# Performance work log

Measured on AMD Instinct MI355X. Metric: run time of the kernel, lower is better.

## Reference

```python
import jax, jax.numpy as jnp
import numpy as np

N_LAYERS = 4
D_MODEL = 256
N_HEADS = 8
D_FF = 2 * D_MODEL
EPS_ATTN = 1e-6
EPS_LN = 1e-5


def setup_inputs() -> dict:
    key = jax.random.key(0)
    ks = jax.random.split(key, 20)
    C, F, L = D_MODEL, D_FF, N_LAYERS
    s = 0.02
    return {
        "ref_feature": jax.random.normal(ks[0], (4, C, 128, 128), jnp.float32),
        # per-layer stacked params (torch nn.Linear convention: y = x @ W.T + b)
        "Wq": jax.random.normal(ks[1], (L, C, C), jnp.float32) * s,
        "bq": jnp.zeros((L, C), jnp.float32),
        "Wk": jax.random.normal(ks[2], (L, C, C), jnp.float32) * s,
        "bk": jnp.zeros((L, C), jnp.float32),
        "Wv": jax.random.normal(ks[3], (L, C, C), jnp.float32) * s,
        "bv": jnp.zeros((L, C), jnp.float32),
        "Wo": jax.random.normal(ks[4], (L, C, C), jnp.float32) * s,
        "bo": jnp.zeros((L, C), jnp.float32),
        "g1": jnp.ones((L, C), jnp.float32),
        "be1": jnp.zeros((L, C), jnp.float32),
        "W1": jax.random.normal(ks[5], (L, F, C), jnp.float32) * s,
        "c1": jnp.zeros((L, F), jnp.float32),
        "W2": jax.random.normal(ks[6], (L, C, F), jnp.float32) * s,
        "c2": jnp.zeros((L, C), jnp.float32),
        "g2": jnp.ones((L, C), jnp.float32),
        "be2": jnp.zeros((L, C), jnp.float32),
    }


def _layer_norm(x, g, b):
    m = jnp.mean(x, axis=-1, keepdims=True)
    v = jnp.mean(jnp.square(x - m), axis=-1, keepdims=True)
    return (x - m) * jax.lax.rsqrt(v + EPS_LN) * g + b


def _feature_map(x):
    return jax.nn.elu(x) + 1.0


def reference(ref_feature, Wq, bq, Wk, bk, Wv, bv, Wo, bo,
              g1, be1, W1, c1, W2, c2, g2, be2):
    N, C, H, W = ref_feature.shape
    Hh, D = N_HEADS, C // N_HEADS
    # patch embed: flatten to tokens [N, HW, C]
    x = ref_feature.reshape(N, C, H * W).transpose(0, 2, 1)

    def body(x, p):
        (Wq_, bq_, Wk_, bk_, Wv_, bv_, Wo_, bo_,
         g1_, be1_, W1_, c1_, W2_, c2_, g2_, be2_) = p
        L = x.shape[1]
        q = (x @ Wq_.T + bq_).reshape(N, L, Hh, D)
        k = (x @ Wk_.T + bk_).reshape(N, L, Hh, D)
        v = (x @ Wv_.T + bv_).reshape(N, L, Hh, D)
        Q = _feature_map(q)
        K = _feature_map(k)
        KV = jnp.einsum('nshd,nshm->nhmd', K, v)            # [N,H,D,D]
        Z = 1.0 / (jnp.einsum('nlhd,nhd->nlh', Q, K.sum(axis=1)) + EPS_ATTN)
        attn = jnp.einsum('nlhd,nhmd,nlh->nlhm', Q, KV, Z).reshape(N, L, C)
        x = _layer_norm(x + attn @ Wo_.T + bo_, g1_, be1_)
        y = jax.nn.relu(x @ W1_.T + c1_) @ W2_.T + c2_
        x = _layer_norm(x + y, g2_, be2_)
        return x, x

    params = (Wq, bq, Wk, bk, Wv, bv, Wo, bo,
              g1, be1, W1, c1, W2, c2, g2, be2)
    _, ys = jax.lax.scan(body, x, params)
    # ys: [n_layers, N, HW, C] -> [n_layers, N, C, H, W]
    return ys.transpose(0, 1, 3, 2).reshape(N_LAYERS, N, C, H, W)
```

## Files before the change

### kernel.cpp

```cpp
#include <hip/hip_runtime.h>
#include <hip/hip_bf16.h>
#include <math.h>

#define NB     4
#define CDIM   256
#define HWDIM  16384
#define LTOK   16384
#define NH     8
#define HD     32
#define FF     512
#define MTOK   (NB * LTOK)
#define NLAYER 4

typedef __bf16 bf16x8 __attribute__((ext_vector_type(8)));
typedef __bf16 bf16x4 __attribute__((ext_vector_type(4)));
typedef float  floatx4 __attribute__((ext_vector_type(4)));

#define GLD16(gp, lp)                                                        \
    __builtin_amdgcn_global_load_lds(                                        \
        (const __attribute__((address_space(1))) void*)(gp),                 \
        (__attribute__((address_space(3))) void*)(lp), 16, 0, 0)

__global__ __launch_bounds__(256)
void f2b_kernel(const float* __restrict__ in, __bf16* __restrict__ out)
{
    int i = (blockIdx.x * 256 + threadIdx.x) * 4;
    float4 f = *(const float4*)&in[i];
    bf16x4 h;
    h[0] = (__bf16)f.x; h[1] = (__bf16)f.y; h[2] = (__bf16)f.z; h[3] = (__bf16)f.w;
    *(bf16x4*)&out[i] = h;
}

__global__ __launch_bounds__(256)
void patch_embed(const float* __restrict__ in, __bf16* __restrict__ out)
{
    __shared__ float tile[32][33];
    const int n = blockIdx.z;
    const int hw0 = blockIdx.x * 32, c0 = blockIdx.y * 32;
    const int tx = threadIdx.x, ty = threadIdx.y;
#pragma unroll
    for (int i = 0; i < 32; i += 8)
        tile[ty + i][tx] = in[(long long)n * CDIM * HWDIM + (long long)(c0 + ty + i) * HWDIM + hw0 + tx];
    __syncthreads();
#pragma unroll
    for (int i = 0; i < 32; i += 8)
        out[(long long)(n * HWDIM + hw0 + ty + i) * CDIM + c0 + tx] = (__bf16)tile[tx][ty + i];
}

__global__ __launch_bounds__(256)
void out_transpose(const __bf16* __restrict__ X, float* __restrict__ out)
{
    __shared__ float tile[32][33];
    const int n = blockIdx.z;
    const int c0 = blockIdx.x * 32, l0 = blockIdx.y * 32;
    const int tid = threadIdx.x;
    {
        int row = tid >> 3, cq = tid & 7;
        bf16x4 x4 = *(const bf16x4*)&X[(long long)(n * LTOK + l0 + row) * CDIM + c0 + cq * 4];
#pragma unroll
        for (int j = 0; j < 4; ++j)
            tile[row][cq * 4 + j] = (float)x4[j];
    }
    __syncthreads();
    {
        int r = tid >> 3, lg = tid & 7;
        float4 o;
        o.x = tile[lg * 4 + 0][r];
        o.y = tile[lg * 4 + 1][r];
        o.z = tile[lg * 4 + 2][r];
        o.w = tile[lg * 4 + 3][r];
        *(float4*)&out[(long long)n * CDIM * LTOK + (long long)(c0 + r) * LTOK + l0 + lg * 4] = o;
    }
}

#define GEMM_STAGE(Aq, Bq, Kdim)                                             \
    __syncthreads();                                                         \
    _Pragma("unroll")                                                        \
    for (int i = 0; i < 4; ++i) {                                            \
        int s = wave * 256 + i * 64 + lane;                                  \
        int row = s >> 3, kq = s & 7;                                        \
        GLD16(&(Aq)[(long long)(m0 + row) * (Kdim) + k0 + kq * 8],           \
              &Asl[(wave * 256 + i * 64) * 8]);                              \
    }                                                                        \
    _Pragma("unroll")                                                        \
    for (int i = 0; i < 4; ++i) {                                            \
        int s = wave * 256 + i * 64 + lane;                                  \
        int row = s >> 3, kq = s & 7;                                        \
        GLD16(&(Bq)[(long long)(n0 + row) * (Kdim) + k0 + kq * 8],           \
              &Bsl[(wave * 256 + i * 64) * 8]);                              \
    }                                                                        \
    __syncthreads();

#define GEMM_MFMA()                                                          \
    _Pragma("unroll")                                                        \
    for (int ko = 0; ko < 2; ++ko) {                                         \
        bf16x8 af[4], bfr[4];                                                \
        _Pragma("unroll")                                                    \
        for (int mt = 0; mt < 4; ++mt)                                       \
            af[mt] = *(const bf16x8*)&Asl[(wm + mt * 16 + l15) * 64 + ko * 32 + quad * 8]; \
        _Pragma("unroll")                                                    \
        for (int nt = 0; nt < 4; ++nt)                                       \
            bfr[nt] = *(const bf16x8*)&Bsl[(wn + nt * 16 + l15) * 64 + ko * 32 + quad * 8]; \
        _Pragma("unroll")                                                    \
        for (int mt = 0; mt < 4; ++mt)                                       \
            _Pragma("unroll")                                                \
            for (int nt = 0; nt < 4; ++nt)                                   \
                acc[mt][nt] = __builtin_amdgcn_mfma_f32_16x16x32_bf16(       \
                    bfr[nt], af[mt], acc[mt][nt], 0, 0, 0);                  \
    }

template <int ACT>
__global__ __launch_bounds__(256)
void gemm_bf16(const __bf16* __restrict__ A, const __bf16* __restrict__ B,
               const float* __restrict__ bias, __bf16* __restrict__ C,
               int M, int K, int O)
{
    __shared__ __bf16 Asl[128 * 64];
    __shared__ __bf16 Bsl[128 * 64];

    const int tid  = threadIdx.x;
    const int lane = tid & 63;
    const int wave = tid >> 6;
    const int m0   = blockIdx.x * 128;
    const int n0   = blockIdx.y * 128;
    const int l15  = lane & 15;
    const int quad = lane >> 4;
    const int wm   = (wave & 1) * 64;
    const int wn   = (wave >> 1) * 64;

    floatx4 acc[4][4];
#pragma unroll
    for (int i = 0; i < 4; ++i)
#pragma unroll
        for (int j = 0; j < 4; ++j)
            acc[i][j] = (floatx4){0.f, 0.f, 0.f, 0.f};

    for (int k0 = 0; k0 < K; k0 += 64) {
        GEMM_STAGE(A, B, K)
        GEMM_MFMA()
    }

#pragma unroll
    for (int mt = 0; mt < 4; ++mt) {
        int row = m0 + wm + mt * 16 + l15;
#pragma unroll
        for (int nt = 0; nt < 4; ++nt) {
            int col0 = n0 + wn + nt * 16 + quad * 4;
            float4 bb = *(const float4*)&bias[col0];
            bf16x4 o;
#pragma unroll
            for (int r = 0; r < 4; ++r) {
                float v = acc[mt][nt][r] + ((r == 0) ? bb.x : (r == 1) ? bb.y : (r == 2) ? bb.z : bb.w);
                if (ACT == 1) v = v > 0.f ? v + 1.f : __expf(v);
                if (ACT == 2) v = v > 0.f ? v : 0.f;
                o[r] = (__bf16)v;
            }
            *(bf16x4*)&C[(long long)row * O + col0] = o;
        }
    }
}

__global__ __launch_bounds__(256)
void gemm_qkv(const __bf16* __restrict__ X,
              const __bf16* __restrict__ Wq, const __bf16* __restrict__ Wk,
              const __bf16* __restrict__ Wv,
              const float* __restrict__ bq, const float* __restrict__ bk,
              const float* __restrict__ bv,
              __bf16* __restrict__ Qo, __bf16* __restrict__ Ko,
              __bf16* __restrict__ Vo)
{
    __shared__ __bf16 Asl[128 * 64];
    __shared__ __bf16 Bsl[128 * 64];

    const int sel = blockIdx.y >> 1;
    const __bf16* B    = (sel == 0) ? Wq : (sel == 1) ? Wk : Wv;
    const float*  bias = (sel == 0) ? bq : (sel == 1) ? bk : bv;
    __bf16*       C    = (sel == 0) ? Qo : (sel == 1) ? Ko : Vo;
    const bool do_elu  = sel < 2;

    const int tid  = threadIdx.x;
    const int lane = tid & 63;
    const int wave = tid >> 6;
    const int m0   = blockIdx.x * 128;
    const int n0   = (blockIdx.y & 1) * 128;
    const int l15  = lane & 15;
    const int quad = lane >> 4;
    const int wm   = (wave & 1) * 64;
    const int wn   = (wave >> 1) * 64;

    floatx4 acc[4][4];
#pragma unroll
    for (int i = 0; i < 4; ++i)
#pragma unroll
        for (int j = 0; j < 4; ++j)
            acc[i][j] = (floatx4){0.f, 0.f, 0.f, 0.f};

    for (int k0 = 0; k0 < CDIM; k0 += 64) {
        GEMM_STAGE(X, B, CDIM)
        GEMM_MFMA()
    }

#pragma unroll
    for (int mt = 0; mt < 4; ++mt) {
        int row = m0 + wm + mt * 16 + l15;
#pragma unroll
        for (int nt = 0; nt < 4; ++nt) {
            int col0 = n0 + wn + nt * 16 + quad * 4;
            float4 bb = *(const float4*)&bias[col0];
            bf16x4 o;
#pragma unroll
            for (int r = 0; r < 4; ++r) {
                float v = acc[mt][nt][r] + ((r == 0) ? bb.x : (r == 1) ? bb.y : (r == 2) ? bb.z : bb.w);
                if (do_elu) v = v > 0.f ? v + 1.f : __expf(v);
                o[r] = (__bf16)v;
            }
            *(bf16x4*)&C[(long long)row * CDIM + col0] = o;
        }
    }
}

__global__ __launch_bounds__(256)
void kv_kernel(const __bf16* __restrict__ Kg, const __bf16* __restrict__ Vg,
               float* __restrict__ KV, float* __restrict__ KS)
{
    __shared__ float Ks[64 * 32];
    __shared__ float Vs[64 * 32];
    const int n = blockIdx.z, h = blockIdx.y;
    const int tid = threadIdx.x;
    const int d  = tid & 31;
    const int m4 = tid >> 5;

    float acc[4] = {0.f, 0.f, 0.f, 0.f};
    float ksum = 0.f;

    for (int sub = 0; sub < 8; ++sub) {
        int s0 = blockIdx.x * 512 + sub * 64;
        __syncthreads();
        {
            int e   = tid * 8;
            int tok = e >> 5, dd = e & 31;
            long long gi = (long long)(n * LTOK + s0 + tok) * CDIM + h * HD + dd;
            bf16x8 kk = *(const bf16x8*)&Kg[gi];
            bf16x8 vv = *(const bf16x8*)&Vg[gi];
#pragma unroll
            for (int j = 0; j < 8; ++j) {
                Ks[e + j] = (float)kk[j];
                Vs[e + j] = (float)vv[j];
            }
        }
        __syncthreads();
#pragma unroll 4
        for (int s = 0; s < 64; ++s) {
            float kd = Ks[s * 32 + d];
            if (m4 == 0) ksum += kd;
#pragma unroll
            for (int j = 0; j < 4; ++j)
                acc[j] += Vs[s * 32 + m4 * 4 + j] * kd;
        }
    }
#pragma unroll
    for (int j = 0; j < 4; ++j)
        atomicAdd(&KV[(((n * NH + h) * HD) + (m4 * 4 + j)) * HD + d], acc[j]);
    if (m4 == 0)
        atomicAdd(&KS[(n * NH + h) * HD + d], ksum);
}

__global__ __launch_bounds__(256)
void attn_kernel(const __bf16* __restrict__ Q, const float* __restrict__ KV,
                 const float* __restrict__ KS, __bf16* __restrict__ out)
{
    __shared__ float q_lds[16 * 256];
    const int n = blockIdx.y;
    const int tid = threadIdx.x;
    const int h = tid >> 5;
    const int m = tid & 31;

    float4 kvr[8], ksr[8];
    {
        const float4* kvp = (const float4*)&KV[(((long long)n * NH + h) * HD + m) * HD];
        const float4* ksp = (const float4*)&KS[((long long)n * NH + h) * HD];
#pragma unroll
        for (int i = 0; i < 8; ++i) { kvr[i] = kvp[i]; ksr[i] = ksp[i]; }
    }

    for (int it = 0; it < 4; ++it) {
        int l0 = blockIdx.x * 64 + it * 16;
        __syncthreads();
#pragma unroll
        for (int i = 0; i < 4; ++i) {
            int e = tid * 4 + i * 1024;
            int row = e >> 8, col = e & 255;
            bf16x4 q4 = *(const bf16x4*)&Q[(long long)(n * LTOK + l0 + row) * CDIM + col];
            float4 f;
            f.x = (float)q4[0]; f.y = (float)q4[1]; f.z = (float)q4[2]; f.w = (float)q4[3];
            *(float4*)&q_lds[e] = f;
        }
        __syncthreads();
#pragma unroll 2
        for (int t = 0; t < 16; ++t) {
            const float4* qr = (const float4*)&q_lds[t * 256 + h * 32];
            float num = 0.f, den = 0.f;
#pragma unroll
            for (int i = 0; i < 8; ++i) {
                float4 q4 = qr[i];
                num += q4.x * kvr[i].x + q4.y * kvr[i].y + q4.z * kvr[i].z + q4.w * kvr[i].w;
                den += q4.x * ksr[i].x + q4.y * ksr[i].y + q4.z * ksr[i].z + q4.w * ksr[i].w;
            }
            out[(long long)(n * LTOK + l0 + t) * CDIM + tid] = (__bf16)(num / (den + 1e-6f));
        }
    }
}

__global__ __launch_bounds__(256)
void ln_kernel(__bf16* __restrict__ X, const __bf16* __restrict__ T,
               const float* __restrict__ g, const float* __restrict__ b)
{
    const int tid  = threadIdx.x;
    const int wave = tid >> 6;
    const int lane = tid & 63;
    const long long tok = (long long)blockIdx.x * 4 + wave;
    const long long base = tok * CDIM + lane * 4;

    bf16x4 xv = *(const bf16x4*)&X[base];
    bf16x4 tv = *(const bf16x4*)&T[base];
    float v[4];
#pragma unroll
    for (int j = 0; j < 4; ++j) v[j] = (float)xv[j] + (float)tv[j];

    float s = v[0] + v[1] + v[2] + v[3];
#pragma unroll
    for (int off = 32; off > 0; off >>= 1) s += __shfl_xor(s, off, 64);
    float mean = s * (1.f / 256.f);

    float dv[4];
    float ss = 0.f;
#pragma unroll
    for (int j = 0; j < 4; ++j) { dv[j] = v[j] - mean; ss += dv[j] * dv[j]; }
#pragma unroll
    for (int off = 32; off > 0; off >>= 1) ss += __shfl_xor(ss, off, 64);
    float rstd = rsqrtf(ss * (1.f / 256.f) + 1e-5f);

    const float4 gv = ((const float4*)g)[lane];
    const float4 bv = ((const float4*)b)[lane];
    bf16x4 o;
    o[0] = (__bf16)(dv[0] * rstd * gv.x + bv.x);
    o[1] = (__bf16)(dv[1] * rstd * gv.y + bv.y);
    o[2] = (__bf16)(dv[2] * rstd * gv.z + bv.z);
    o[3] = (__bf16)(dv[3] * rstd * gv.w + bv.w);
    *(bf16x4*)&X[base] = o;
}

extern "C" void kernel_launch(void* const* d_in, const int* in_sizes, int n_in,
                              void* d_out, int out_size, void* d_ws, size_t ws_size,
                              hipStream_t stream)
{
    const float* ref = (const float*)d_in[0];
    const float* Wq  = (const float*)d_in[1];  const float* bq = (const float*)d_in[2];
    const float* Wk  = (const float*)d_in[3];  const float* bk = (const float*)d_in[4];
    const float* Wv  = (const float*)d_in[5];  const float* bv = (const float*)d_in[6];
    const float* Wo  = (const float*)d_in[7];  const float* bo = (const float*)d_in[8];
    const float* g1  = (const float*)d_in[9];  const float* be1 = (const float*)d_in[10];
    const float* W1  = (const float*)d_in[11]; const float* c1 = (const float*)d_in[12];
    const float* W2  = (const float*)d_in[13]; const float* c2 = (const float*)d_in[14];
    const float* g2  = (const float*)d_in[15]; const float* be2 = (const float*)d_in[16];
    float* out = (float*)d_out;

    const size_t SZ = (size_t)MTOK * CDIM;
    __bf16* Xb = (__bf16*)d_ws;
    __bf16* Qb = Xb + SZ;
    __bf16* Kb = Qb + SZ;
    __bf16* Vb = Kb + SZ;
    __bf16* Hb = Vb + SZ;
    float*  KVb = (float*)(Hb + 2 * SZ);
    float*  KSb = KVb + NB * NH * HD * HD;
    __bf16* Wqb = (__bf16*)(KSb + NB * NH * HD);
    const size_t WC = (size_t)NLAYER * CDIM * CDIM;
    const size_t WF = (size_t)NLAYER * FF * CDIM;
    __bf16* Wkb = Wqb + WC;
    __bf16* Wvb = Wkb + WC;
    __bf16* Wob = Wvb + WC;
    __bf16* W1b = Wob + WC;
    __bf16* W2b = W1b + WF;

    f2b_kernel<<<WC / 1024, 256, 0, stream>>>(Wq, Wqb);
    f2b_kernel<<<WC / 1024, 256, 0, stream>>>(Wk, Wkb);
    f2b_kernel<<<WC / 1024, 256, 0, stream>>>(Wv, Wvb);
    f2b_kernel<<<WC / 1024, 256, 0, stream>>>(Wo, Wob);
    f2b_kernel<<<WF / 1024, 256, 0, stream>>>(W1, W1b);
    f2b_kernel<<<WF / 1024, 256, 0, stream>>>(W2, W2b);

    dim3 tb(32, 8);
    patch_embed<<<dim3(HWDIM / 32, CDIM / 32, NB), tb, 0, stream>>>(ref, Xb);

    for (int l = 0; l < NLAYER; ++l) {
        const __bf16* Wq_l = Wqb + (size_t)l * CDIM * CDIM;
        const __bf16* Wk_l = Wkb + (size_t)l * CDIM * CDIM;
        const __bf16* Wv_l = Wvb + (size_t)l * CDIM * CDIM;
        const __bf16* Wo_l = Wob + (size_t)l * CDIM * CDIM;
        const __bf16* W1_l = W1b + (size_t)l * FF * CDIM;
        const __bf16* W2_l = W2b + (size_t)l * CDIM * FF;
        const float* bq_l = bq + (size_t)l * CDIM;
        const float* bk_l = bk + (size_t)l * CDIM;
        const float* bv_l = bv + (size_t)l * CDIM;
        const float* bo_l = bo + (size_t)l * CDIM;
        const float* c1_l = c1 + (size_t)l * FF;
        const float* c2_l = c2 + (size_t)l * CDIM;
        const float* g1_l = g1 + (size_t)l * CDIM;
        const float* g2_l = g2 + (size_t)l * CDIM;
        const float* be1_l = be1 + (size_t)l * CDIM;
        const float* be2_l = be2 + (size_t)l * CDIM;

        dim3 gC(MTOK / 128, CDIM / 128);
        dim3 gF(MTOK / 128, FF / 128);

        gemm_qkv<<<dim3(MTOK / 128, 6), 256, 0, stream>>>(
            Xb, Wq_l, Wk_l, Wv_l, bq_l, bk_l, bv_l, Qb, Kb, Vb);

        hipMemsetAsync(KVb, 0, (NB * NH * HD * HD + NB * NH * HD) * sizeof(float), stream);
        kv_kernel<<<dim3(LTOK / 512, NH, NB), 256, 0, stream>>>(Kb, Vb, KVb, KSb);

        attn_kernel<<<dim3(LTOK / 64, NB), 256, 0, stream>>>(Qb, KVb, KSb, Kb);
        gemm_bf16<0><<<gC, 256, 0, stream>>>(Kb, Wo_l, bo_l, Vb, MTOK, CDIM, CDIM);

        ln_kernel<<<MTOK / 4, 256, 0, stream>>>(Xb, Vb, g1_l, be1_l);

        gemm_bf16<2><<<gF, 256, 0, stream>>>(Xb, W1_l, c1_l, Hb, MTOK, CDIM, FF);
        gemm_bf16<0><<<gC, 256, 0, stream>>>(Hb, W2_l, c2_l, Vb, MTOK, FF, CDIM);

        ln_kernel<<<MTOK / 4, 256, 0, stream>>>(Xb, Vb, g2_l, be2_l);

        out_transpose<<<dim3(CDIM / 32, LTOK / 32, NB), 256, 0, stream>>>(
            Xb, out + (size_t)l * NB * CDIM * LTOK);
    }
}
```

Measured before the change: 1.657 ms.

## Widen GEMM tiles to full 256 columns and fuse residual+LayerNorm into epilogue

GEMM tiles grow from 128x128 to 128x256, so each block covers a full 256-wide output row. That lets the Wo and W2 GEMMs add the residual, compute LayerNorm statistics with a cross-wave LDS reduction and write normalized X in place, which removes two separate LN kernels and the Vb round trip per layer. QKV and FFN1 also use the wider tiles to cut redundant A-tile reloads. The cost is higher register pressure (a 4x8 accumulator array) and fewer blocks. Variance is now computed as E[x^2]-mean^2 in fp32, which is slightly less numerically robust.

```diff
diff --git a/kernel.cpp b/kernel.cpp
--- a/kernel.cpp
+++ b/kernel.cpp
@@ -73,94 +73,59 @@
     }
 }
 
-#define GEMM_STAGE(Aq, Bq, Kdim)                                             \
+#define WIDE_PROLOGUE()                                                      \
+    const int tid  = threadIdx.x;                                            \
+    const int lane = tid & 63;                                               \
+    const int wave = tid >> 6;                                               \
+    const int m0   = blockIdx.x * 128;                                       \
+    const int l15  = lane & 15;                                              \
+    const int quad = lane >> 4;                                              \
+    const int wm   = (wave & 1) * 64;                                        \
+    const int wn   = (wave >> 1) * 128;                                      \
+    floatx4 acc[4][8];                                                       \
+    _Pragma("unroll")                                                        \
+    for (int i = 0; i < 4; ++i)                                              \
+        _Pragma("unroll")                                                    \
+        for (int j = 0; j < 8; ++j)                                          \
+            acc[i][j] = (floatx4){0.f, 0.f, 0.f, 0.f};
+
+#define WIDE_STAGE(Aq, Bq, KD)                                               \
     __syncthreads();                                                         \
     _Pragma("unroll")                                                        \
     for (int i = 0; i < 4; ++i) {                                            \
         int s = wave * 256 + i * 64 + lane;                                  \
         int row = s >> 3, kq = s & 7;                                        \
-        GLD16(&(Aq)[(long long)(m0 + row) * (Kdim) + k0 + kq * 8],           \
+        GLD16(&(Aq)[(long long)(m0 + row) * (KD) + k0 + kq * 8],             \
               &Asl[(wave * 256 + i * 64) * 8]);                              \
     }                                                                        \
     _Pragma("unroll")                                                        \
-    for (int i = 0; i < 4; ++i) {                                            \
-        int s = wave * 256 + i * 64 + lane;                                  \
+    for (int i = 0; i < 8; ++i) {                                            \
+        int s = wave * 512 + i * 64 + lane;                                  \
         int row = s >> 3, kq = s & 7;                                        \
-        GLD16(&(Bq)[(long long)(n0 + row) * (Kdim) + k0 + kq * 8],           \
-              &Bsl[(wave * 256 + i * 64) * 8]);                              \
+        GLD16(&(Bq)[(long long)row * (KD) + k0 + kq * 8],                    \
+              &Bsl[(wave * 512 + i * 64) * 8]);                              \
     }                                                                        \
     __syncthreads();
 
-#define GEMM_MFMA()                                                          \
+#define WIDE_MFMA()                                                          \
     _Pragma("unroll")                                                        \
     for (int ko = 0; ko < 2; ++ko) {                                         \
-        bf16x8 af[4], bfr[4];                                                \
+        bf16x8 af[4], bfr[8];                                                \
         _Pragma("unroll")                                                    \
         for (int mt = 0; mt < 4; ++mt)                                       \
             af[mt] = *(const bf16x8*)&Asl[(wm + mt * 16 + l15) * 64 + ko * 32 + quad * 8]; \
         _Pragma("unroll")                                                    \
-        for (int nt = 0; nt < 4; ++nt)                                       \
+        for (int nt = 0; nt < 8; ++nt)                                       \
             bfr[nt] = *(const bf16x8*)&Bsl[(wn + nt * 16 + l15) * 64 + ko * 32 + quad * 8]; \
         _Pragma("unroll")                                                    \
         for (int mt = 0; mt < 4; ++mt)                                       \
             _Pragma("unroll")                                                \
-            for (int nt = 0; nt < 4; ++nt)                                   \
+            for (int nt = 0; nt < 8; ++nt)                                   \
                 acc[mt][nt] = __builtin_amdgcn_mfma_f32_16x16x32_bf16(       \
                     bfr[nt], af[mt], acc[mt][nt], 0, 0, 0);                  \
     }
 
-template <int ACT>
-__global__ __launch_bounds__(256)
-void gemm_bf16(const __bf16* __restrict__ A, const __bf16* __restrict__ B,
-               const float* __restrict__ bias, __bf16* __restrict__ C,
-               int M, int K, int O)
-{
-    __shared__ __bf16 Asl[128 * 64];
-    __shared__ __bf16 Bsl[128 * 64];
-
-    const int tid  = threadIdx.x;
-    const int lane = tid & 63;
-    const int wave = tid >> 6;
-    const int m0   = blockIdx.x * 128;
-    const int n0   = blockIdx.y * 128;
-    const int l15  = lane & 15;
-    const int quad = lane >> 4;
-    const int wm   = (wave & 1) * 64;
-    const int wn   = (wave >> 1) * 64;
-
-    floatx4 acc[4][4];
-#pragma unroll
-    for (int i = 0; i < 4; ++i)
-#pragma unroll
-        for (int j = 0; j < 4; ++j)
-            acc[i][j] = (floatx4){0.f, 0.f, 0.f, 0.f};
-
-    for (int k0 = 0; k0 < K; k0 += 64) {
-        GEMM_STAGE(A, B, K)
-        GEMM_MFMA()
-    }
-
-#pragma unroll
-    for (int mt = 0; mt < 4; ++mt) {
-        int row = m0 + wm + mt * 16 + l15;
-#pragma unroll
-        for (int nt = 0; nt < 4; ++nt) {
-            int col0 = n0 + wn + nt * 16 + quad * 4;
-            float4 bb = *(const float4*)&bias[col0];
-            bf16x4 o;
-#pragma unroll
-            for (int r = 0; r < 4; ++r) {
-                float v = acc[mt][nt][r] + ((r == 0) ? bb.x : (r == 1) ? bb.y : (r == 2) ? bb.z : bb.w);
-                if (ACT == 1) v = v > 0.f ? v + 1.f : __expf(v);
-                if (ACT == 2) v = v > 0.f ? v : 0.f;
-                o[r] = (__bf16)v;
-            }
-            *(bf16x4*)&C[(long long)row * O + col0] = o;
-        }
-    }
-}
-
-__global__ __launch_bounds__(256)
+__global__ __launch_bounds__(256, 2)
 void gemm_qkv(const __bf16* __restrict__ X,
               const __bf16* __restrict__ Wq, const __bf16* __restrict__ Wk,
               const __bf16* __restrict__ Wv,
@@ -170,42 +135,24 @@
               __bf16* __restrict__ Vo)
 {
     __shared__ __bf16 Asl[128 * 64];
-    __shared__ __bf16 Bsl[128 * 64];
-
-    const int sel = blockIdx.y >> 1;
+    __shared__ __bf16 Bsl[256 * 64];
+    const int sel = blockIdx.y;
     const __bf16* B    = (sel == 0) ? Wq : (sel == 1) ? Wk : Wv;
     const float*  bias = (sel == 0) ? bq : (sel == 1) ? bk : bv;
     __bf16*       C    = (sel == 0) ? Qo : (sel == 1) ? Ko : Vo;
     const bool do_elu  = sel < 2;
 
-    const int tid  = threadIdx.x;
-    const int lane = tid & 63;
-    const int wave = tid >> 6;
-    const int m0   = blockIdx.x * 128;
-    const int n0   = (blockIdx.y & 1) * 128;
-    const int l15  = lane & 15;
-    const int quad = lane >> 4;
-    const int wm   = (wave & 1) * 64;
-    const int wn   = (wave >> 1) * 64;
-
-    floatx4 acc[4][4];
-#pragma unroll
-    for (int i = 0; i < 4; ++i)
-#pragma unroll
-        for (int j = 0; j < 4; ++j)
-            acc[i][j] = (floatx4){0.f, 0.f, 0.f, 0.f};
-
+    WIDE_PROLOGUE()
     for (int k0 = 0; k0 < CDIM; k0 += 64) {
-        GEMM_STAGE(X, B, CDIM)
-        GEMM_MFMA()
-    }
-
+        WIDE_STAGE(X, B, CDIM)
+        WIDE_MFMA()
+    }
 #pragma unroll
     for (int mt = 0; mt < 4; ++mt) {
         int row = m0 + wm + mt * 16 + l15;
 #pragma unroll
-        for (int nt = 0; nt < 4; ++nt) {
-            int col0 = n0 + wn + nt * 16 + quad * 4;
+        for (int nt = 0; nt < 8; ++nt) {
+            int col0 = wn + nt * 16 + quad * 4;
             float4 bb = *(const float4*)&bias[col0];
             bf16x4 o;
 #pragma unroll
@@ -215,6 +162,121 @@
                 o[r] = (__bf16)v;
             }
             *(bf16x4*)&C[(long long)row * CDIM + col0] = o;
+        }
+    }
+}
+
+__global__ __launch_bounds__(256, 2)
+void gemm_relu(const __bf16* __restrict__ A, const __bf16* __restrict__ Bw,
+               const float* __restrict__ bias, __bf16* __restrict__ C)
+{
+    __shared__ __bf16 Asl[128 * 64];
+    __shared__ __bf16 Bsl[256 * 64];
+    const int n_base = blockIdx.y * 256;
+    const __bf16* B = Bw + (long long)n_base * CDIM;
+
+    WIDE_PROLOGUE()
+    for (int k0 = 0; k0 < CDIM; k0 += 64) {
+        WIDE_STAGE(A, B, CDIM)
+        WIDE_MFMA()
+    }
+#pragma unroll
+    for (int mt = 0; mt < 4; ++mt) {
+        int row = m0 + wm + mt * 16 + l15;
+#pragma unroll
+        for (int nt = 0; nt < 8; ++nt) {
+            int col0 = wn + nt * 16 + quad * 4;
+            float4 bb = *(const float4*)&bias[n_base + col0];
+            bf16x4 o;
+#pragma unroll
+            for (int r = 0; r < 4; ++r) {
+                float v = acc[mt][nt][r] + ((r == 0) ? bb.x : (r == 1) ? bb.y : (r == 2) ? bb.z : bb.w);
+                o[r] = (__bf16)(v > 0.f ? v : 0.f);
+            }
+            *(bf16x4*)&C[(long long)row * FF + n_base + col0] = o;
+        }
+    }
+}
+
+template <int KDIM>
+__global__ __launch_bounds__(256, 2)
+void gemm_ln(const __bf16* __restrict__ A, const __bf16* __restrict__ B,
+             const float* __restrict__ bias, __bf16* X,
+             const float* __restrict__ g, const float* __restrict__ be)
+{
+    __shared__ __bf16 Asl[128 * 64];
+    __shared__ __bf16 Bsl[256 * 64];
+
+    WIDE_PROLOGUE()
+    for (int k0 = 0; k0 < KDIM; k0 += 64) {
+        WIDE_STAGE(A, B, KDIM)
+        WIDE_MFMA()
+    }
+
+#pragma unroll
+    for (int mt = 0; mt < 4; ++mt) {
+        int row = m0 + wm + mt * 16 + l15;
+#pragma unroll
+        for (int nt = 0; nt < 8; ++nt) {
+            int col0 = wn + nt * 16 + quad * 4;
+            float4 bb = *(const float4*)&bias[col0];
+            bf16x4 xr = *(const bf16x4*)&X[(long long)row * CDIM + col0];
+            acc[mt][nt][0] += bb.x + (float)xr[0];
+            acc[mt][nt][1] += bb.y + (float)xr[1];
+            acc[mt][nt][2] += bb.z + (float)xr[2];
+            acc[mt][nt][3] += bb.w + (float)xr[3];
+        }
+    }
+
+    float psum[4], psq[4];
+#pragma unroll
+    for (int mt = 0; mt < 4; ++mt) {
+        float s = 0.f, q = 0.f;
+#pragma unroll
+        for (int nt = 0; nt < 8; ++nt)
+#pragma unroll
+            for (int r = 0; r < 4; ++r) {
+                float v = acc[mt][nt][r];
+                s += v; q += v * v;
+            }
+        s += __shfl_xor(s, 16, 64); s += __shfl_xor(s, 32, 64);
+        q += __shfl_xor(q, 16, 64); q += __shfl_xor(q, 32, 64);
+        psum[mt] = s; psq[mt] = q;
+    }
+
+    float* red = (float*)Asl;
+    const int half = wave >> 1;
+    __syncthreads();
+    if (quad == 0) {
+#pragma unroll
+        for (int mt = 0; mt < 4; ++mt) {
+            int rl = wm + mt * 16 + l15;
+            red[rl * 4 + half * 2 + 0] = psum[mt];
+            red[rl * 4 + half * 2 + 1] = psq[mt];
+        }
+    }
+    __syncthreads();
+
+#pragma unroll
+    for (int mt = 0; mt < 4; ++mt) {
+        int rl  = wm + mt * 16 + l15;
+        float tot = red[rl * 4 + 0] + red[rl * 4 + 2];
+        float tsq = red[rl * 4 + 1] + red[rl * 4 + 3];
+        float mean = tot * (1.f / 256.f);
+        float var  = tsq * (1.f / 256.f) - mean * mean;
+        float rstd = rsqrtf(var + 1e-5f);
+        int row = m0 + rl;
+#pragma unroll
+        for (int nt = 0; nt < 8; ++nt) {
+            int col0 = wn + nt * 16 + quad * 4;
+            float4 gg = *(const float4*)&g[col0];
+            float4 ee = *(const float4*)&be[col0];
+            bf16x4 o;
+            o[0] = (__bf16)((acc[mt][nt][0] - mean) * rstd * gg.x + ee.x);
+            o[1] = (__bf16)((acc[mt][nt][1] - mean) * rstd * gg.y + ee.y);
+            o[2] = (__bf16)((acc[mt][nt][2] - mean) * rstd * gg.z + ee.z);
+            o[3] = (__bf16)((acc[mt][nt][3] - mean) * rstd * gg.w + ee.w);
+            *(bf16x4*)&X[(long long)row * CDIM + col0] = o;
         }
     }
 }
@@ -309,45 +371,6 @@
             out[(long long)(n * LTOK + l0 + t) * CDIM + tid] = (__bf16)(num / (den + 1e-6f));
         }
     }
-}
-
-__global__ __launch_bounds__(256)
-void ln_kernel(__bf16* __restrict__ X, const __bf16* __restrict__ T,
-               const float* __restrict__ g, const float* __restrict__ b)
-{
-    const int tid  = threadIdx.x;
-    const int wave = tid >> 6;
-    const int lane = tid & 63;
-    const long long tok = (long long)blockIdx.x * 4 + wave;
-    const long long base = tok * CDIM + lane * 4;
-
-    bf16x4 xv = *(const bf16x4*)&X[base];
-    bf16x4 tv = *(const bf16x4*)&T[base];
-    float v[4];
-#pragma unroll
-    for (int j = 0; j < 4; ++j) v[j] = (float)xv[j] + (float)tv[j];
-
-    float s = v[0] + v[1] + v[2] + v[3];
-#pragma unroll
-    for (int off = 32; off > 0; off >>= 1) s += __shfl_xor(s, off, 64);
-    float mean = s * (1.f / 256.f);
-
-    float dv[4];
-    float ss = 0.f;
-#pragma unroll
-    for (int j = 0; j < 4; ++j) { dv[j] = v[j] - mean; ss += dv[j] * dv[j]; }
-#pragma unroll
-    for (int off = 32; off > 0; off >>= 1) ss += __shfl_xor(ss, off, 64);
-    float rstd = rsqrtf(ss * (1.f / 256.f) + 1e-5f);
-
-    const float4 gv = ((const float4*)g)[lane];
-    const float4 bv = ((const float4*)b)[lane];
-    bf16x4 o;
-    o[0] = (__bf16)(dv[0] * rstd * gv.x + bv.x);
-    o[1] = (__bf16)(dv[1] * rstd * gv.y + bv.y);
-    o[2] = (__bf16)(dv[2] * rstd * gv.z + bv.z);
-    o[3] = (__bf16)(dv[3] * rstd * gv.w + bv.w);
-    *(bf16x4*)&X[base] = o;
 }
 
 extern "C" void kernel_launch(void* const* d_in, const int* in_sizes, int n_in,
@@ -410,24 +433,19 @@
         const float* be1_l = be1 + (size_t)l * CDIM;
         const float* be2_l = be2 + (size_t)l * CDIM;
 
-        dim3 gC(MTOK / 128, CDIM / 128);
-        dim3 gF(MTOK / 128, FF / 128);
-
-        gemm_qkv<<<dim3(MTOK / 128, 6), 256, 0, stream>>>(
+        gemm_qkv<<<dim3(MTOK / 128, 3), 256, 0, stream>>>(
             Xb, Wq_l, Wk_l, Wv_l, bq_l, bk_l, bv_l, Qb, Kb, Vb);
 
         hipMemsetAsync(KVb, 0, (NB * NH * HD * HD + NB * NH * HD) * sizeof(float), stream);
         kv_kernel<<<dim3(LTOK / 512, NH, NB), 256, 0, stream>>>(Kb, Vb, KVb, KSb);
 
         attn_kernel<<<dim3(LTOK / 64, NB), 256, 0, stream>>>(Qb, KVb, KSb, Kb);
-        gemm_bf16<0><<<gC, 256, 0, stream>>>(Kb, Wo_l, bo_l, Vb, MTOK, CDIM, CDIM);
-
-        ln_kernel<<<MTOK / 4, 256, 0, stream>>>(Xb, Vb, g1_l, be1_l);
-
-        gemm_bf16<2><<<gF, 256, 0, stream>>>(Xb, W1_l, c1_l, Hb, MTOK, CDIM, FF);
-        gemm_bf16<0><<<gC, 256, 0, stream>>>(Hb, W2_l, c2_l, Vb, MTOK, FF, CDIM);
-
-        ln_kernel<<<MTOK / 4, 256, 0, stream>>>(Xb, Vb, g2_l, be2_l);
+
+        gemm_ln<CDIM><<<MTOK / 128, 256, 0, stream>>>(Kb, Wo_l, bo_l, Xb, g1_l, be1_l);
+
+        gemm_relu<<<dim3(MTOK / 128, 2), 256, 0, stream>>>(Xb, W1_l, c1_l, Hb);
+
+        gemm_ln<FF><<<MTOK / 128, 256, 0, stream>>>(Hb, W2_l, c2_l, Xb, g2_l, be2_l);
 
         out_transpose<<<dim3(CDIM / 32, LTOK / 32, NB), 256, 0, stream>>>(
             Xb, out + (size_t)l * NB * CDIM * LTOK);
```

New measurement: 1.455 ms. 12.2% less time.
